# Kernel tuning notes

Hardware: AMD Instinct MI355X
Metric: run time of the kernel (lower is better)

## Reference

```python
import jax, jax.numpy as jnp
import numpy as np


def setup_inputs() -> dict:
    key = jax.random.key(0)
    ks = jax.random.split(key, 8)
    B, C, W = 8, 512, 2048
    Cq = C // 8
    sq = 1.0 / np.sqrt(C)
    return {
        "x": jax.random.normal(ks[0], (B, C, W), dtype=jnp.float32),
        "Wq": jax.random.normal(ks[1], (Cq, C), dtype=jnp.float32) * sq,
        "bq": jax.random.normal(ks[2], (Cq,), dtype=jnp.float32) * 0.01,
        "Wk": jax.random.normal(ks[3], (Cq, C), dtype=jnp.float32) * sq,
        "bk": jax.random.normal(ks[4], (Cq,), dtype=jnp.float32) * 0.01,
        "Wv": jax.random.normal(ks[5], (C, C), dtype=jnp.float32) * sq,
        "bv": jax.random.normal(ks[6], (C,), dtype=jnp.float32) * 0.01,
        "gamma": jax.random.normal(ks[7], (1,), dtype=jnp.float32),
    }


def reference(x, Wq, bq, Wk, bk, Wv, bv, gamma):
    # x: [B, C, W]; 1x1 Conv1d == channel-mixing matmul.
    q = jnp.einsum("qc,bcw->bqw", Wq, x) + bq[None, :, None]   # [B, C/8, W]
    k = jnp.einsum("qc,bcw->bqw", Wk, x) + bk[None, :, None]   # [B, C/8, W]
    v = jnp.einsum("oc,bcw->bow", Wv, x) + bv[None, :, None]   # [B, C, W]
    # energy[b, i, j] = sum_q q[b, q, i] * k[b, q, j]  (query positions i attend over j)
    energy = jnp.einsum("bqi,bqj->bij", q, k)                  # [B, W, W]
    attn = jax.nn.softmax(energy, axis=-1)                     # [B, W, W]
    # out[b, c, i] = sum_j v[b, c, j] * attn[b, i, j]
    out = jnp.einsum("bcj,bij->bci", v, attn)                  # [B, C, W]
    return gamma[0] * out + x
```

## Files before the change

kernel.cpp:

```cpp
#include <hip/hip_runtime.h>

#define B_  8
#define C_  512
#define CQ_ 64
#define W_  2048
#define NROW 640

typedef __attribute__((ext_vector_type(8))) short  short8;
typedef __attribute__((ext_vector_type(4))) float  f32x4;
typedef unsigned short ushort;
typedef unsigned long long ull;

static constexpr size_t OFF_VB  = 0;
static constexpr size_t OFF_QTH = OFF_VB  + (size_t)B_ * C_ * W_ / 2;
static constexpr size_t OFF_QTL = OFF_QTH + (size_t)B_ * W_ * CQ_ / 2;
static constexpr size_t OFF_KTH = OFF_QTL + (size_t)B_ * W_ * CQ_ / 2;
static constexpr size_t OFF_KTL = OFF_KTH + (size_t)B_ * W_ * CQ_ / 2;
static constexpr size_t OFF_XTH = OFF_KTL + (size_t)B_ * W_ * CQ_ / 2;
static constexpr size_t OFF_XTL = OFF_XTH + (size_t)B_ * W_ * C_ / 2;
static constexpr size_t OFF_WH  = OFF_XTL + (size_t)B_ * W_ * C_ / 2;
static constexpr size_t OFF_WL  = OFF_WH  + (size_t)NROW * C_ / 2;

static __device__ __forceinline__ ushort f2bf(float f) {
    unsigned int u = __builtin_bit_cast(unsigned int, f);
    u += 0x7fffu + ((u >> 16) & 1u);
    return (ushort)(u >> 16);
}
static __device__ __forceinline__ float bf2f(ushort h) {
    unsigned int u = ((unsigned int)h) << 16;
    return __builtin_bit_cast(float, u);
}
static __device__ __forceinline__ ull pack4(const ushort* p) {
    return (ull)p[0] | ((ull)p[1] << 16) | ((ull)p[2] << 32) | ((ull)p[3] << 48);
}

__global__ __launch_bounds__(256) void k_wsplit(
    const float* __restrict__ Wq, const float* __restrict__ Wk,
    const float* __restrict__ Wv, ushort* __restrict__ wh, ushort* __restrict__ wl)
{
    const int idx = (blockIdx.x * 256 + threadIdx.x) * 4;
    const int row = idx >> 9, col = idx & 511;
    const float* src;
    if (row < 64)       src = Wq + (size_t)row * C_ + col;
    else if (row < 128) src = Wk + (size_t)(row - 64) * C_ + col;
    else                src = Wv + (size_t)(row - 128) * C_ + col;
    float4 v = *reinterpret_cast<const float4*>(src);
    float vv[4] = {v.x, v.y, v.z, v.w};
    ushort h[4], lo[4];
    #pragma unroll
    for (int j = 0; j < 4; ++j) {
        h[j]  = f2bf(vv[j]);
        lo[j] = f2bf(vv[j] - bf2f(h[j]));
    }
    *reinterpret_cast<ull*>(wh + idx) = pack4(h);
    *reinterpret_cast<ull*>(wl + idx) = pack4(lo);
}

__global__ __launch_bounds__(256) void k_xt(
    const float* __restrict__ x, ushort* __restrict__ xth, ushort* __restrict__ xtl)
{
    const int b = blockIdx.z, c0 = blockIdx.y * 64, w0 = blockIdx.x * 64;
    __shared__ float ts[64][65];
    const int t = threadIdx.x;
    #pragma unroll
    for (int m = 0; m < 4; ++m) {
        int fi = m * 256 + t;
        int c = fi >> 4, c4 = fi & 15;
        float4 v = *reinterpret_cast<const float4*>(x + ((size_t)b * C_ + c0 + c) * W_ + w0 + c4 * 4);
        ts[c][c4 * 4 + 0] = v.x; ts[c][c4 * 4 + 1] = v.y;
        ts[c][c4 * 4 + 2] = v.z; ts[c][c4 * 4 + 3] = v.w;
    }
    __syncthreads();
    #pragma unroll
    for (int m = 0; m < 4; ++m) {
        int w  = m * 16 + (t >> 4);
        int cc = (t & 15) * 4;
        ushort h[4], lo[4];
        #pragma unroll
        for (int j = 0; j < 4; ++j) {
            float v = ts[cc + j][w];
            h[j]  = f2bf(v);
            lo[j] = f2bf(v - bf2f(h[j]));
        }
        size_t base = ((size_t)b * W_ + w0 + w) * C_ + c0 + cc;
        *reinterpret_cast<ull*>(xth + base) = pack4(h);
        *reinterpret_cast<ull*>(xtl + base) = pack4(lo);
    }
}

__global__ __launch_bounds__(512) void k_projm(
    const ushort* __restrict__ wh, const ushort* __restrict__ wl,
    const ushort* __restrict__ xth, const ushort* __restrict__ xtl,
    const float* __restrict__ bq, const float* __restrict__ bk,
    const float* __restrict__ bv,
    ushort* __restrict__ qth, ushort* __restrict__ qtl,
    ushort* __restrict__ kth, ushort* __restrict__ ktl,
    ushort* __restrict__ vb)
{
    const int b = blockIdx.y, w0 = blockIdx.x * 64;
    const int t = threadIdx.x, l = t & 63, wid = t >> 6;
    const int lr = l & 15, lkb = (l >> 4) * 8;

    f32x4 acc[5][4];
    #pragma unroll
    for (int m = 0; m < 5; ++m)
        #pragma unroll
        for (int n = 0; n < 4; ++n) acc[m][n] = (f32x4){0.f, 0.f, 0.f, 0.f};

    const size_t xbase = ((size_t)b * W_ + w0 + lr) * C_ + lkb;

    for (int kc = 0; kc < 16; ++kc) {
        short8 bhf[4], blf[4];
        #pragma unroll
        for (int n = 0; n < 4; ++n) {
            bhf[n] = *reinterpret_cast<const short8*>(xth + xbase + (size_t)n * 16 * C_ + kc * 32);
            blf[n] = *reinterpret_cast<const short8*>(xtl + xbase + (size_t)n * 16 * C_ + kc * 32);
        }
        #pragma unroll
        for (int m = 0; m < 5; ++m) {
            const int arow = (wid + m * 8) * 16 + lr;
            const size_t abase = (size_t)arow * C_ + kc * 32 + lkb;
            short8 ah = *reinterpret_cast<const short8*>(wh + abase);
            #pragma unroll
            for (int n = 0; n < 4; ++n)
                acc[m][n] = __builtin_amdgcn_mfma_f32_16x16x32_bf16(ah, bhf[n], acc[m][n], 0, 0, 0);
            if (m == 0) {
                short8 al = *reinterpret_cast<const short8*>(wl + abase);
                #pragma unroll
                for (int n = 0; n < 4; ++n) {
                    acc[m][n] = __builtin_amdgcn_mfma_f32_16x16x32_bf16(al, bhf[n], acc[m][n], 0, 0, 0);
                    acc[m][n] = __builtin_amdgcn_mfma_f32_16x16x32_bf16(ah, blf[n], acc[m][n], 0, 0, 0);
                }
            }
        }
    }

    #pragma unroll
    for (int m = 0; m < 5; ++m) {
        const int rbase16 = (wid + m * 8) * 16;
        if (rbase16 < 128) {
            ushort* oh = (rbase16 < 64) ? qth : kth;
            ushort* ol = (rbase16 < 64) ? qtl : ktl;
            const float* bias = (rbase16 < 64) ? bq : bk;
            const int rb = rbase16 & 63;
            #pragma unroll
            for (int n = 0; n < 4; ++n) {
                const int wcol = w0 + n * 16 + lr;
                ushort h4[4], l4[4];
                #pragma unroll
                for (int r = 0; r < 4; ++r) {
                    const int rowl = rb + (l >> 4) * 4 + r;
                    float val = acc[m][n][r] + bias[rowl];
                    h4[r] = f2bf(val);
                    l4[r] = f2bf(val - bf2f(h4[r]));
                }
                size_t base = ((size_t)b * W_ + wcol) * CQ_ + rb + (l >> 4) * 4;
                *reinterpret_cast<ull*>(oh + base) = pack4(h4);
                *reinterpret_cast<ull*>(ol + base) = pack4(l4);
            }
        } else {
            #pragma unroll
            for (int n = 0; n < 4; ++n) {
                const int wcol = w0 + n * 16 + lr;
                #pragma unroll
                for (int r = 0; r < 4; ++r) {
                    const int rl = rbase16 - 128 + (l >> 4) * 4 + r;
                    vb[((size_t)b * C_ + rl) * W_ + wcol] = f2bf(acc[m][n][r] + bv[rl]);
                }
            }
        }
    }
}

__global__ __launch_bounds__(512) void k_flash(
    const ushort* __restrict__ qth, const ushort* __restrict__ qtl,
    const ushort* __restrict__ kth, const ushort* __restrict__ ktl,
    const ushort* __restrict__ vb,
    const float* __restrict__ x, const float* __restrict__ gamma,
    float* __restrict__ out)
{
    const int b  = blockIdx.y;
    const int i0 = blockIdx.x * 64;
    const int t = threadIdx.x, l = t & 63, wid = t >> 6;
    const int lr = l & 15, lkb = (l >> 4) * 8;
    const int ib = (wid & 3) * 16;

    __shared__ __align__(16) ushort Ps[64 * 64];
    __shared__ float scale_lds[64];
    __shared__ float l_lds[64];

    short8 qh[2], ql[2];
    if (wid < 4) {
        const size_t qbase = ((size_t)b * W_ + i0 + ib + lr) * CQ_ + lkb;
        #pragma unroll
        for (int kc = 0; kc < 2; ++kc) {
            qh[kc] = *reinterpret_cast<const short8*>(qth + qbase + kc * 32);
            ql[kc] = *reinterpret_cast<const short8*>(qtl + qbase + kc * 32);
        }
    }

    f32x4 acc[4][4];
    #pragma unroll
    for (int i = 0; i < 4; ++i)
        #pragma unroll
        for (int j = 0; j < 4; ++j) acc[i][j] = (f32x4){0.f, 0.f, 0.f, 0.f};

    float mrun[4] = {-3.0e38f, -3.0e38f, -3.0e38f, -3.0e38f};
    float lrun[4] = {0.f, 0.f, 0.f, 0.f};

    const ushort* vbase = vb + ((size_t)b * C_ + wid * 64) * W_;

    for (int jt = 0; jt < 32; ++jt) {
        const int j0 = jt * 64;

        if (wid < 4) {
            f32x4 e[4];
            #pragma unroll
            for (int n = 0; n < 4; ++n) e[n] = (f32x4){0.f, 0.f, 0.f, 0.f};
            #pragma unroll
            for (int kc = 0; kc < 2; ++kc) {
                short8 bh[4], bl[4];
                #pragma unroll
                for (int n = 0; n < 4; ++n) {
                    const size_t ka = ((size_t)b * W_ + j0 + n * 16 + lr) * CQ_ + kc * 32 + lkb;
                    bh[n] = *reinterpret_cast<const short8*>(kth + ka);
                    bl[n] = *reinterpret_cast<const short8*>(ktl + ka);
                }
                #pragma unroll
                for (int n = 0; n < 4; ++n) {
                    e[n] = __builtin_amdgcn_mfma_f32_16x16x32_bf16(qh[kc], bh[n], e[n], 0, 0, 0);
                    e[n] = __builtin_amdgcn_mfma_f32_16x16x32_bf16(ql[kc], bh[n], e[n], 0, 0, 0);
                    e[n] = __builtin_amdgcn_mfma_f32_16x16x32_bf16(qh[kc], bl[n], e[n], 0, 0, 0);
                }
            }
            float rmax[4];
            #pragma unroll
            for (int r = 0; r < 4; ++r)
                rmax[r] = fmaxf(fmaxf(e[0][r], e[1][r]), fmaxf(e[2][r], e[3][r]));
            #pragma unroll
            for (int off = 1; off <= 8; off <<= 1)
                #pragma unroll
                for (int r = 0; r < 4; ++r)
                    rmax[r] = fmaxf(rmax[r], __shfl_xor(rmax[r], off));
            float sc[4];
            #pragma unroll
            for (int r = 0; r < 4; ++r) {
                const float mnew = fmaxf(mrun[r], rmax[r]);
                sc[r] = __expf(mrun[r] - mnew);
                mrun[r] = mnew;
            }
            float rsum[4] = {0.f, 0.f, 0.f, 0.f};
            #pragma unroll
            for (int n = 0; n < 4; ++n)
                #pragma unroll
                for (int r = 0; r < 4; ++r) {
                    const float p = __expf(e[n][r] - mrun[r]);
                    e[n][r] = p;
                    rsum[r] += p;
                }
            #pragma unroll
            for (int off = 1; off <= 8; off <<= 1)
                #pragma unroll
                for (int r = 0; r < 4; ++r)
                    rsum[r] += __shfl_xor(rsum[r], off);
            #pragma unroll
            for (int r = 0; r < 4; ++r)
                lrun[r] = lrun[r] * sc[r] + rsum[r];
            #pragma unroll
            for (int n = 0; n < 4; ++n)
                #pragma unroll
                for (int r = 0; r < 4; ++r) {
                    const int row = ib + (l >> 4) * 4 + r;
                    const int idx = (row * 64 + n * 16 + lr) ^ ((row & 7) << 3);
                    Ps[idx] = f2bf(e[n][r]);
                }
            if (lr == 0) {
                #pragma unroll
                for (int r = 0; r < 4; ++r)
                    scale_lds[ib + (l >> 4) * 4 + r] = sc[r];
            }
        }
        __syncthreads();

        float s4[4];
        #pragma unroll
        for (int fi = 0; fi < 4; ++fi) s4[fi] = scale_lds[fi * 16 + lr];
        #pragma unroll
        for (int fc = 0; fc < 4; ++fc)
            #pragma unroll
            for (int fi = 0; fi < 4; ++fi)
                acc[fc][fi] *= s4[fi];
        #pragma unroll
        for (int kc = 0; kc < 2; ++kc) {
            short8 a[4], p[4];
            #pragma unroll
            for (int f = 0; f < 4; ++f) {
                a[f] = *reinterpret_cast<const short8*>(vbase + (size_t)(f * 16 + lr) * W_ + j0 + kc * 32 + lkb);
                const int row = f * 16 + lr;
                const int idx = ((row * 64) + kc * 32 + lkb) ^ ((row & 7) << 3);
                p[f] = *reinterpret_cast<const short8*>(&Ps[idx]);
            }
            #pragma unroll
            for (int fc = 0; fc < 4; ++fc)
                #pragma unroll
                for (int fi = 0; fi < 4; ++fi)
                    acc[fc][fi] = __builtin_amdgcn_mfma_f32_16x16x32_bf16(a[fc], p[fi], acc[fc][fi], 0, 0, 0);
        }
        __syncthreads();
    }

    if (wid < 4 && lr == 0) {
        #pragma unroll
        for (int r = 0; r < 4; ++r)
            l_lds[ib + (l >> 4) * 4 + r] = lrun[r];
    }
    __syncthreads();
    float linv[4];
    #pragma unroll
    for (int fi = 0; fi < 4; ++fi) linv[fi] = 1.0f / l_lds[fi * 16 + lr];

    const float g = gamma[0];
    #pragma unroll
    for (int fc = 0; fc < 4; ++fc) {
        const int c = wid * 64 + fc * 16 + (l >> 4) * 4;
        #pragma unroll
        for (int fi = 0; fi < 4; ++fi) {
            const int icol = i0 + fi * 16 + lr;
            #pragma unroll
            for (int r = 0; r < 4; ++r) {
                const size_t addr = ((size_t)b * C_ + c + r) * W_ + icol;
                out[addr] = g * acc[fc][fi][r] * linv[fi] + x[addr];
            }
        }
    }
}

extern "C" void kernel_launch(void* const* d_in, const int* in_sizes, int n_in,
                              void* d_out, int out_size, void* d_ws, size_t ws_size,
                              hipStream_t stream)
{
    const float* x     = (const float*)d_in[0];
    const float* Wq    = (const float*)d_in[1];
    const float* bq    = (const float*)d_in[2];
    const float* Wk    = (const float*)d_in[3];
    const float* bk    = (const float*)d_in[4];
    const float* Wv    = (const float*)d_in[5];
    const float* bv    = (const float*)d_in[6];
    const float* gamma = (const float*)d_in[7];
    float* out = (float*)d_out;
    float* ws  = (float*)d_ws;

    ushort* vbf = (ushort*)(ws + OFF_VB);
    ushort* qth = (ushort*)(ws + OFF_QTH);
    ushort* qtl = (ushort*)(ws + OFF_QTL);
    ushort* kth = (ushort*)(ws + OFF_KTH);
    ushort* ktl = (ushort*)(ws + OFF_KTL);
    ushort* xth = (ushort*)(ws + OFF_XTH);
    ushort* xtl = (ushort*)(ws + OFF_XTL);
    ushort* wh  = (ushort*)(ws + OFF_WH);
    ushort* wl  = (ushort*)(ws + OFF_WL);

    hipLaunchKernelGGL(k_wsplit, dim3(NROW * C_ / 1024, 1, 1), dim3(256), 0, stream,
                       Wq, Wk, Wv, wh, wl);
    hipLaunchKernelGGL(k_xt,     dim3(W_ / 64, C_ / 64, B_), dim3(256), 0, stream,
                       x, xth, xtl);
    hipLaunchKernelGGL(k_projm,  dim3(W_ / 64, B_, 1), dim3(512), 0, stream,
                       wh, wl, xth, xtl, bq, bk, bv, qth, qtl, kth, ktl, vbf);
    hipLaunchKernelGGL(k_flash,  dim3(W_ / 64, B_, 1), dim3(512), 0, stream,
                       qth, qtl, kth, ktl, vbf, x, gamma, out);
}
```

Measured before the change: 314.5 us.

## Warp-specialize flash kernel with double-buffered P tiles and producer/consumer overlap

Splits the flash-attention block into producer waves, which compute QK^T, the online softmax and P tiles into two alternating LDS buffers, and consumer waves, which run the PV MFMAs over 128 channels each. The two groups work one tile apart so softmax and PV overlap. K fragments and V tiles are prefetched a step ahead, and rescaling of the accumulator is skipped when no row max changed. The grid is flattened with batch as the fast index, and launch bounds ask for 2 blocks per CU. The risks are higher register pressure from the 8x4 accumulators in consumer waves, and producer work now runs on only half the waves.

New measurement: 344.3 us. 1.09x slower.

```diff
diff --git a/kernel.cpp b/kernel.cpp
--- a/kernel.cpp
+++ b/kernel.cpp
@@ -172,67 +172,62 @@
     }
 }
 
-__global__ __launch_bounds__(512) void k_flash(
+__global__ __launch_bounds__(512, 2) void k_flash(
     const ushort* __restrict__ qth, const ushort* __restrict__ qtl,
     const ushort* __restrict__ kth, const ushort* __restrict__ ktl,
     const ushort* __restrict__ vb,
     const float* __restrict__ x, const float* __restrict__ gamma,
     float* __restrict__ out)
 {
-    const int b  = blockIdx.y;
-    const int i0 = blockIdx.x * 64;
+    const int b  = blockIdx.x & 7;
+    const int i0 = (blockIdx.x >> 3) * 64;
     const int t = threadIdx.x, l = t & 63, wid = t >> 6;
     const int lr = l & 15, lkb = (l >> 4) * 8;
-    const int ib = (wid & 3) * 16;
-
-    __shared__ __align__(16) ushort Ps[64 * 64];
-    __shared__ float scale_lds[64];
-    __shared__ float l_lds[64];
-
-    short8 qh[2], ql[2];
+
+    __shared__ __align__(16) ushort Ps0[64 * 64];
+    __shared__ __align__(16) ushort Ps1[64 * 64];
+    __shared__ float sc0[64], sc1[64], l_lds[64];
+    __shared__ int   fl0[4], fl1[4];
+
     if (wid < 4) {
-        const size_t qbase = ((size_t)b * W_ + i0 + ib + lr) * CQ_ + lkb;
-        #pragma unroll
-        for (int kc = 0; kc < 2; ++kc) {
-            qh[kc] = *reinterpret_cast<const short8*>(qth + qbase + kc * 32);
-            ql[kc] = *reinterpret_cast<const short8*>(qtl + qbase + kc * 32);
-        }
-    }
-
-    f32x4 acc[4][4];
-    #pragma unroll
-    for (int i = 0; i < 4; ++i)
-        #pragma unroll
-        for (int j = 0; j < 4; ++j) acc[i][j] = (f32x4){0.f, 0.f, 0.f, 0.f};
-
-    float mrun[4] = {-3.0e38f, -3.0e38f, -3.0e38f, -3.0e38f};
-    float lrun[4] = {0.f, 0.f, 0.f, 0.f};
-
-    const ushort* vbase = vb + ((size_t)b * C_ + wid * 64) * W_;
-
-    for (int jt = 0; jt < 32; ++jt) {
-        const int j0 = jt * 64;
-
-        if (wid < 4) {
+        const int ib = wid * 16;
+        short8 qh[2], ql[2];
+        {
+            const size_t qbase = ((size_t)b * W_ + i0 + ib + lr) * CQ_ + lkb;
+            #pragma unroll
+            for (int kc = 0; kc < 2; ++kc) {
+                qh[kc] = *reinterpret_cast<const short8*>(qth + qbase + kc * 32);
+                ql[kc] = *reinterpret_cast<const short8*>(qtl + qbase + kc * 32);
+            }
+        }
+        float mrun[4] = {-3.0e38f, -3.0e38f, -3.0e38f, -3.0e38f};
+        float lrun[4] = {0.f, 0.f, 0.f, 0.f};
+
+        short8 khA[2][4], klA[2][4], khB[2][4], klB[2][4];
+
+        auto LOADK = [&](short8 kh[2][4], short8 kl[2][4], int tjt) {
+            #pragma unroll
+            for (int kc = 0; kc < 2; ++kc)
+                #pragma unroll
+                for (int n = 0; n < 4; ++n) {
+                    const size_t ka = ((size_t)b * W_ + tjt * 64 + n * 16 + lr) * CQ_ + kc * 32 + lkb;
+                    kh[kc][n] = *reinterpret_cast<const short8*>(kth + ka);
+                    kl[kc][n] = *reinterpret_cast<const short8*>(ktl + ka);
+                }
+        };
+        auto QKSTEP = [&](short8 kh[2][4], short8 kl[2][4],
+                          ushort* PsX, float* scX, int* flX) {
             f32x4 e[4];
             #pragma unroll
             for (int n = 0; n < 4; ++n) e[n] = (f32x4){0.f, 0.f, 0.f, 0.f};
             #pragma unroll
-            for (int kc = 0; kc < 2; ++kc) {
-                short8 bh[4], bl[4];
+            for (int kc = 0; kc < 2; ++kc)
                 #pragma unroll
                 for (int n = 0; n < 4; ++n) {
-                    const size_t ka = ((size_t)b * W_ + j0 + n * 16 + lr) * CQ_ + kc * 32 + lkb;
-                    bh[n] = *reinterpret_cast<const short8*>(kth + ka);
-                    bl[n] = *reinterpret_cast<const short8*>(ktl + ka);
-                }
-                #pragma unroll
-                for (int n = 0; n < 4; ++n) {
-                    e[n] = __builtin_amdgcn_mfma_f32_16x16x32_bf16(qh[kc], bh[n], e[n], 0, 0, 0);
-                    e[n] = __builtin_amdgcn_mfma_f32_16x16x32_bf16(ql[kc], bh[n], e[n], 0, 0, 0);
-                    e[n] = __builtin_amdgcn_mfma_f32_16x16x32_bf16(qh[kc], bl[n], e[n], 0, 0, 0);
-                }
-            }
+                    e[n] = __builtin_amdgcn_mfma_f32_16x16x32_bf16(qh[kc], kh[kc][n], e[n], 0, 0, 0);
+                    e[n] = __builtin_amdgcn_mfma_f32_16x16x32_bf16(ql[kc], kh[kc][n], e[n], 0, 0, 0);
+                    e[n] = __builtin_amdgcn_mfma_f32_16x16x32_bf16(qh[kc], kl[kc][n], e[n], 0, 0, 0);
+                }
             float rmax[4];
             #pragma unroll
             for (int r = 0; r < 4; ++r)
@@ -242,12 +237,14 @@
                 #pragma unroll
                 for (int r = 0; r < 4; ++r)
                     rmax[r] = fmaxf(rmax[r], __shfl_xor(rmax[r], off));
-            float sc[4];
+            float scr[4];
+            bool upd = false;
             #pragma unroll
             for (int r = 0; r < 4; ++r) {
                 const float mnew = fmaxf(mrun[r], rmax[r]);
-                sc[r] = __expf(mrun[r] - mnew);
+                scr[r] = __expf(mrun[r] - mnew);
                 mrun[r] = mnew;
+                upd = upd || (scr[r] != 1.0f);
             }
             float rsum[4] = {0.f, 0.f, 0.f, 0.f};
             #pragma unroll
@@ -265,71 +262,143 @@
                     rsum[r] += __shfl_xor(rsum[r], off);
             #pragma unroll
             for (int r = 0; r < 4; ++r)
-                lrun[r] = lrun[r] * sc[r] + rsum[r];
+                lrun[r] = lrun[r] * scr[r] + rsum[r];
             #pragma unroll
             for (int n = 0; n < 4; ++n)
                 #pragma unroll
                 for (int r = 0; r < 4; ++r) {
                     const int row = ib + (l >> 4) * 4 + r;
                     const int idx = (row * 64 + n * 16 + lr) ^ ((row & 7) << 3);
-                    Ps[idx] = f2bf(e[n][r]);
+                    PsX[idx] = f2bf(e[n][r]);
                 }
             if (lr == 0) {
                 #pragma unroll
                 for (int r = 0; r < 4; ++r)
-                    scale_lds[ib + (l >> 4) * 4 + r] = sc[r];
-            }
-        }
+                    scX[ib + (l >> 4) * 4 + r] = scr[r];
+            }
+            const ull ba = __ballot(upd);
+            if (l == 0) flX[wid] = (ba != 0ull) ? 1 : 0;
+        };
+
+        LOADK(khA, klA, 0);
+        QKSTEP(khA, klA, Ps0, sc0, fl0);
+        LOADK(khB, klB, 1);
         __syncthreads();
 
-        float s4[4];
-        #pragma unroll
-        for (int fi = 0; fi < 4; ++fi) s4[fi] = scale_lds[fi * 16 + lr];
-        #pragma unroll
-        for (int fc = 0; fc < 4; ++fc)
+        for (int jt2 = 0; jt2 < 32; jt2 += 2) {
+            {
+                const int tp = jt2 + 1;
+                if (tp < 32) {
+                    if (jt2 + 2 < 32) LOADK(khA, klA, jt2 + 2);
+                    QKSTEP(khB, klB, Ps1, sc1, fl1);
+                }
+                __syncthreads();
+            }
+            {
+                const int tp = jt2 + 2;
+                if (tp < 32) {
+                    if (jt2 + 3 < 32) LOADK(khB, klB, jt2 + 3);
+                    QKSTEP(khA, klA, Ps0, sc0, fl0);
+                }
+                __syncthreads();
+            }
+        }
+        if (lr == 0) {
+            #pragma unroll
+            for (int r = 0; r < 4; ++r)
+                l_lds[ib + (l >> 4) * 4 + r] = lrun[r];
+        }
+        __syncthreads();
+    } else {
+        const int c0w = (wid - 4) * 128;
+        const ushort* vbase = vb + ((size_t)b * C_ + c0w) * W_;
+
+        f32x4 acc[8][4];
+        #pragma unroll
+        for (int fc = 0; fc < 8; ++fc)
+            #pragma unroll
+            for (int fi = 0; fi < 4; ++fi) acc[fc][fi] = (f32x4){0.f, 0.f, 0.f, 0.f};
+
+        int pidx[2][4];
+        #pragma unroll
+        for (int kc = 0; kc < 2; ++kc)
+            #pragma unroll
+            for (int fi = 0; fi < 4; ++fi) {
+                const int row = fi * 16 + lr;
+                pidx[kc][fi] = ((row * 64) + kc * 32 + lkb) ^ ((row & 7) << 3);
+            }
+
+        short8 vpre[8];
+        #pragma unroll
+        for (int fc = 0; fc < 8; ++fc)
+            vpre[fc] = *reinterpret_cast<const short8*>(vbase + (size_t)(fc * 16 + lr) * W_ + 0 + lkb);
+        __syncthreads();
+
+        auto CONSUME = [&](const ushort* PsX, const float* scX, const int* flX, int jt) {
+            const int j0 = jt * 64;
+            short8 vk1[8];
+            #pragma unroll
+            for (int fc = 0; fc < 8; ++fc)
+                vk1[fc] = *reinterpret_cast<const short8*>(vbase + (size_t)(fc * 16 + lr) * W_ + j0 + 32 + lkb);
+            const bool dor = (flX[0] | flX[1] | flX[2] | flX[3]) != 0;
+            if (dor) {
+                float s4[4];
+                #pragma unroll
+                for (int fi = 0; fi < 4; ++fi) s4[fi] = scX[fi * 16 + lr];
+                #pragma unroll
+                for (int fc = 0; fc < 8; ++fc)
+                    #pragma unroll
+                    for (int fi = 0; fi < 4; ++fi)
+                        acc[fc][fi] *= s4[fi];
+            }
+            short8 p0[4], p1[4];
             #pragma unroll
             for (int fi = 0; fi < 4; ++fi)
-                acc[fc][fi] *= s4[fi];
-        #pragma unroll
-        for (int kc = 0; kc < 2; ++kc) {
-            short8 a[4], p[4];
-            #pragma unroll
-            for (int f = 0; f < 4; ++f) {
-                a[f] = *reinterpret_cast<const short8*>(vbase + (size_t)(f * 16 + lr) * W_ + j0 + kc * 32 + lkb);
-                const int row = f * 16 + lr;
-                const int idx = ((row * 64) + kc * 32 + lkb) ^ ((row & 7) << 3);
-                p[f] = *reinterpret_cast<const short8*>(&Ps[idx]);
-            }
-            #pragma unroll
-            for (int fc = 0; fc < 4; ++fc)
+                p0[fi] = *reinterpret_cast<const short8*>(&PsX[pidx[0][fi]]);
+            #pragma unroll
+            for (int fc = 0; fc < 8; ++fc)
                 #pragma unroll
                 for (int fi = 0; fi < 4; ++fi)
-                    acc[fc][fi] = __builtin_amdgcn_mfma_f32_16x16x32_bf16(a[fc], p[fi], acc[fc][fi], 0, 0, 0);
+                    acc[fc][fi] = __builtin_amdgcn_mfma_f32_16x16x32_bf16(vpre[fc], p0[fi], acc[fc][fi], 0, 0, 0);
+            #pragma unroll
+            for (int fi = 0; fi < 4; ++fi)
+                p1[fi] = *reinterpret_cast<const short8*>(&PsX[pidx[1][fi]]);
+            #pragma unroll
+            for (int fc = 0; fc < 8; ++fc)
+                #pragma unroll
+                for (int fi = 0; fi < 4; ++fi)
+                    acc[fc][fi] = __builtin_amdgcn_mfma_f32_16x16x32_bf16(vk1[fc], p1[fi], acc[fc][fi], 0, 0, 0);
+            if (jt + 1 < 32) {
+                #pragma unroll
+                for (int fc = 0; fc < 8; ++fc)
+                    vpre[fc] = *reinterpret_cast<const short8*>(vbase + (size_t)(fc * 16 + lr) * W_ + j0 + 64 + lkb);
+            }
+        };
+
+        for (int jt2 = 0; jt2 < 32; jt2 += 2) {
+            CONSUME(Ps0, sc0, fl0, jt2);
+            __syncthreads();
+            CONSUME(Ps1, sc1, fl1, jt2 + 1);
+            __syncthreads();
         }
         __syncthreads();
-    }
-
-    if (wid < 4 && lr == 0) {
-        #pragma unroll
-        for (int r = 0; r < 4; ++r)
-            l_lds[ib + (l >> 4) * 4 + r] = lrun[r];
-    }
-    __syncthreads();
-    float linv[4];
-    #pragma unroll
-    for (int fi = 0; fi < 4; ++fi) linv[fi] = 1.0f / l_lds[fi * 16 + lr];
-
-    const float g = gamma[0];
-    #pragma unroll
-    for (int fc = 0; fc < 4; ++fc) {
-        const int c = wid * 64 + fc * 16 + (l >> 4) * 4;
-        #pragma unroll
-        for (int fi = 0; fi < 4; ++fi) {
-            const int icol = i0 + fi * 16 + lr;
-            #pragma unroll
-            for (int r = 0; r < 4; ++r) {
-                const size_t addr = ((size_t)b * C_ + c + r) * W_ + icol;
-                out[addr] = g * acc[fc][fi][r] * linv[fi] + x[addr];
+
+        float linv[4];
+        #pragma unroll
+        for (int fi = 0; fi < 4; ++fi) linv[fi] = 1.0f / l_lds[fi * 16 + lr];
+
+        const float g = gamma[0];
+        #pragma unroll
+        for (int fc = 0; fc < 8; ++fc) {
+            const int c = c0w + fc * 16 + (l >> 4) * 4;
+            #pragma unroll
+            for (int fi = 0; fi < 4; ++fi) {
+                const int icol = i0 + fi * 16 + lr;
+                #pragma unroll
+                for (int r = 0; r < 4; ++r) {
+                    const size_t addr = ((size_t)b * C_ + c + r) * W_ + icol;
+                    out[addr] = g * acc[fc][fi][r] * linv[fi] + x[addr];
+                }
             }
         }
     }
@@ -366,6 +435,6 @@
                        x, xth, xtl);
     hipLaunchKernelGGL(k_projm,  dim3(W_ / 64, B_, 1), dim3(512), 0, stream,
                        wh, wl, xth, xtl, bq, bk, bv, qth, qtl, kth, ktl, vbf);
-    hipLaunchKernelGGL(k_flash,  dim3(W_ / 64, B_, 1), dim3(512), 0, stream,
+    hipLaunchKernelGGL(k_flash,  dim3(W_ / 64 * B_, 1, 1), dim3(512), 0, stream,
                        qth, qtl, kth, ktl, vbf, x, gamma, out);
 }
```
